# Performance work log

Measured on AMD Instinct MI355X. Metric: run time of the kernel, lower is better.

The kernel has to match this reference:

```python
import jax, jax.numpy as jnp
import numpy as np

NCONF, NATOMS, NCOEFF = 64, 256, 45
NAOV = 12  # 4 p-vectors + 8 d-vectors (3 'diagonal' + 5 'off-diagonal' rows)

# hyperparameters (floats from the forward signature, fixed here)
LOW_S, UP_S = 0.5, 3.5
LOW_R, UP_R = 0.5, 3.5
LOW_A, UP_A = 0.5, 3.5
LOW_Z, UP_Z = 0.19634954, 2.94524311  # ~pi/16 .. 15*pi/16
OETA_S, OETA_R, OETA_A, OZETA = 16.0, 16.0, 8.0, 32.0


def setup_inputs() -> dict:
    key = jax.random.key(0)
    coefficients = jax.random.normal(key, (NCONF, NATOMS, NCOEFF), dtype=jnp.float32)
    return {"coefficients": coefficients, "NOShfS": 16, "NOShfR": 16, "NOShfA": 8, "NOShfZ": 8}


def _orbital_matrix(coefficients):
    n, a, _ = coefficients.shape
    p = coefficients[:, :, 9:21].reshape(n, a, 4, 3)
    d = coefficients[:, :, 21:45].reshape(n, a, 4, 6)
    d = d[..., jnp.array([0, 2, 5, 4, 3, 1])].reshape(n, a, 8, 3)
    # cat([p, d[:, :, :3], d[:, :, 3:]]) == cat([p, d])
    return jnp.concatenate([p, d], axis=2)  # [n, a, 12, 3]


def reference(coefficients, NOShfS, NOShfR, NOShfA, NOShfZ):
    # basis_functions='spd', use_simple_orbital_aev=False, use_angular_info=True
    n, a, _ = coefficients.shape
    om = _orbital_matrix(coefficients)                 # [n, a, 12, 3]
    dist = jnp.linalg.norm(om, axis=-1)                # [n, a, 12]

    shfS = jnp.linspace(LOW_S, UP_S, NOShfS)
    shfR = jnp.linspace(LOW_R, UP_R, NOShfR)
    s_aev = jnp.exp(-OETA_S * (dist[..., None] - shfS) ** 2)   # [n, a, 12, S]
    r_aev = jnp.exp(-OETA_R * (dist[..., None] - shfR) ** 2)   # [n, a, 12, R]
    radial = jnp.concatenate([s_aev, r_aev], axis=-1).reshape(n, a, NAOV * (NOShfS + NOShfR))

    # angles between all AOV pairs (vectorized version of the nested i<j loop)
    zero_mask = jnp.all(jnp.abs(om) < 1e-12, axis=-1)          # [n, a, 12]
    safe_d = jnp.where(zero_mask, 1.0, dist)
    nv = jnp.where(zero_mask[..., None], 0.0, om / safe_d[..., None])  # normalized AOVs
    iu, ju = np.triu_indices(NAOV, k=1)                        # 66 pairs, i-major order
    cos_ang = jnp.einsum('napk,napk->nap', nv[:, :, iu], nv[:, :, ju])  # [n, a, 66]
    angles = jnp.arccos(0.95 * cos_ang)
    avdist = 0.5 * (dist[:, :, iu] + dist[:, :, ju])           # [n, a, 66]

    shfZ = jnp.linspace(LOW_Z, UP_Z, NOShfZ)
    shfA = jnp.linspace(LOW_A, UP_A, NOShfA)
    factor1 = ((1.0 + jnp.cos(angles[..., None] - shfZ)) * 0.5) ** OZETA      # [n, a, 66, Z]
    factor2 = jnp.exp(-OETA_A * (avdist[..., None] - shfA) ** 2)              # [n, a, 66, A]
    angular = 2.0 * factor1[..., :, None] * factor2[..., None, :]             # [n, a, 66, Z, A]
    angular = angular.reshape(n, a, angles.shape[2] * NOShfZ * NOShfA)

    return jnp.concatenate([radial, angular], axis=-1)  # [n, a, 12*(S+R) + 66*Z*A]
```

## Files before the change

### kernel.cpp

```cpp
#include <hip/hip_runtime.h>
#include <math.h>

#define NCONF  64
#define NATOMS 256
#define NCOEFF 45
#define NAOV   12
#define NPAIR  66
#define NZ     8
#define NA     8
#define RAD    384
#define ANG    4224
#define TOT    4608

__constant__ unsigned char c_iu[NPAIR] = {
    0,0,0,0,0,0,0,0,0,0,0,
    1,1,1,1,1,1,1,1,1,1,
    2,2,2,2,2,2,2,2,2,
    3,3,3,3,3,3,3,3,
    4,4,4,4,4,4,4,
    5,5,5,5,5,5,
    6,6,6,6,6,
    7,7,7,7,
    8,8,8,
    9,9,
    10
};
__constant__ unsigned char c_ju[NPAIR] = {
    1,2,3,4,5,6,7,8,9,10,11,
    2,3,4,5,6,7,8,9,10,11,
    3,4,5,6,7,8,9,10,11,
    4,5,6,7,8,9,10,11,
    5,6,7,8,9,10,11,
    6,7,8,9,10,11,
    7,8,9,10,11,
    8,9,10,11,
    9,10,11,
    10,11,
    11
};

__constant__ float c_shfS[16] = {
    0.5f, 0.7f, 0.9f, 1.1f, 1.3f, 1.5f, 1.7f, 1.9f,
    2.1f, 2.3f, 2.5f, 2.7f, 2.9f, 3.1f, 3.3f, 3.5f
};
__constant__ float c_shfA[8] = {
    0.5f, 0.92857142857f, 1.35714285714f, 1.78571428571f,
    2.21428571429f, 2.64285714286f, 3.07142857143f, 3.5f
};
__constant__ float c_cosZ[8] = {
     0.98078528f,  0.83146961f,  0.55557023f,  0.19509032f,
    -0.19509032f, -0.55557023f, -0.83146961f, -0.98078528f
};
__constant__ float c_sinZ[8] = {
    0.19509032f, 0.55557023f, 0.83146961f, 0.98078528f,
    0.98078528f, 0.83146961f, 0.55557023f, 0.19509032f
};


__global__ __launch_bounds__(256)
void OrbitalAEVComputer_40492951667225_kernel(const float* __restrict__ coef,
                                              float* __restrict__ out) {
    const int atom = blockIdx.x;
    const float* c = coef + (size_t)atom * NCOEFF;
    float* o = out + (size_t)atom * TOT;
    const int t = threadIdx.x;

    __shared__ float s_dist[NAOV];
    __shared__ float s_nv[NAOV][3];
    __shared__ float s_c95[NPAIR];
    __shared__ float s_sin[NPAIR];
    __shared__ float s_avd[NPAIR];
    __shared__ float s_f1[NPAIR * NZ];
    __shared__ float s_f2[NPAIR * NA];

    if (t < NAOV) {
        float x, y, z;
        if (t < 4) {
            x = c[9 + 3 * t]; y = c[10 + 3 * t]; z = c[11 + 3 * t];
        } else {
            int r = (t - 4) >> 1, h = (t - 4) & 1;
            const int base = 21 + 6 * r;
            if (h == 0) { x = c[base + 0]; y = c[base + 2]; z = c[base + 5]; }
            else        { x = c[base + 4]; y = c[base + 3]; z = c[base + 1]; }
        }
        float d = sqrtf(x * x + y * y + z * z);
        bool zm = (fabsf(x) < 1e-12f) && (fabsf(y) < 1e-12f) && (fabsf(z) < 1e-12f);
        float inv = zm ? 0.0f : 1.0f / d;
        s_dist[t] = d;
        s_nv[t][0] = x * inv;
        s_nv[t][1] = y * inv;
        s_nv[t][2] = z * inv;
    }
    __syncthreads();

    if (t < NPAIR) {
        int i = c_iu[t], j = c_ju[t];
        float cang = s_nv[i][0] * s_nv[j][0]
                   + s_nv[i][1] * s_nv[j][1]
                   + s_nv[i][2] * s_nv[j][2];
        float c95 = 0.95f * cang;
        s_c95[t] = c95;
        s_sin[t] = sqrtf(fmaxf(1.0f - c95 * c95, 0.0f));
        s_avd[t] = 0.5f * (s_dist[i] + s_dist[j]);
    }
    __syncthreads();

    for (int idx = t; idx < NPAIR * NZ; idx += 256) {
        int q = idx >> 3, k = idx & 7;
        float cosa = fmaf(s_c95[q], c_cosZ[k], s_sin[q] * c_sinZ[k]);
        float x = 0.5f * (1.0f + cosa);
        x = x * x; x = x * x; x = x * x; x = x * x; x = x * x;
        s_f1[idx] = x;
        float dd = s_avd[q] - c_shfA[k];
        s_f2[idx] = __expf(-8.0f * dd * dd);
    }
    __syncthreads();

    if (t < 96) {
        int e = t * 4;
        int p = e >> 5;
        float d = s_dist[p];
        int k0 = e & 31;
        float4 v;
        {
            float df = d - c_shfS[(k0 + 0) & 15]; v.x = __expf(-16.0f * df * df);
        }
        {
            float df = d - c_shfS[(k0 + 1) & 15]; v.y = __expf(-16.0f * df * df);
        }
        {
            float df = d - c_shfS[(k0 + 2) & 15]; v.z = __expf(-16.0f * df * df);
        }
        {
            float df = d - c_shfS[(k0 + 3) & 15]; v.w = __expf(-16.0f * df * df);
        }
        reinterpret_cast<float4*>(o)[t] = v;
    }

    for (int idx4 = t; idx4 < ANG / 4; idx4 += 256) {
        int e = idx4 * 4;
        int q = e >> 6;
        int z = (e >> 3) & 7;
        int a0 = e & 7;
        float f1 = 2.0f * s_f1[q * 8 + z];
        const float* f2 = &s_f2[q * 8 + a0];
        float4 v;
        v.x = f1 * f2[0];
        v.y = f1 * f2[1];
        v.z = f1 * f2[2];
        v.w = f1 * f2[3];
        reinterpret_cast<float4*>(o + RAD)[idx4] = v;
    }
}

extern "C" void kernel_launch(void* const* d_in, const int* in_sizes, int n_in,
                              void* d_out, int out_size, void* d_ws, size_t ws_size,
                              hipStream_t stream) {
    const float* coef = (const float*)d_in[0];
    float* out = (float*)d_out;
    OrbitalAEVComputer_40492951667225_kernel<<<dim3(NCONF * NATOMS), dim3(256), 0, stream>>>(coef, out);
}
```

Before: 312.1 us.

## Map one atom per wavefront and replace block barriers with wave-local LDS fences

Each 256-thread block now handles four atoms, one per 64-lane wavefront, with per-wave shared-memory slices. The block-wide __syncthreads calls are replaced by s_waitcnt lgkmcnt(0), relying on lockstep execution within a wavefront. The sine is recomputed per element rather than stored, and f2 is read as float4 from LDS. This removes block barrier overhead and idle threads in the small setup phases, but relies on implicit wave synchronicity and does more work per lane in the store loops.

After: 313.4 us. No clear change (+0.4%).

```diff
diff --git a/kernel.cpp b/kernel.cpp
--- a/kernel.cpp
+++ b/kernel.cpp
@@ -11,6 +11,7 @@
 #define RAD    384
 #define ANG    4224
 #define TOT    4608
+#define ATOMS_PER_BLOCK 4
 
 __constant__ unsigned char c_iu[NPAIR] = {
     0,0,0,0,0,0,0,0,0,0,0,
@@ -56,29 +57,32 @@
     0.98078528f, 0.83146961f, 0.55557023f, 0.19509032f
 };
 
+#define WAVE_FENCE() asm volatile("s_waitcnt lgkmcnt(0)" ::: "memory")
+
 
 __global__ __launch_bounds__(256)
 void OrbitalAEVComputer_40492951667225_kernel(const float* __restrict__ coef,
                                               float* __restrict__ out) {
-    const int atom = blockIdx.x;
+    __shared__ __align__(16) float s_f1[ATOMS_PER_BLOCK][NPAIR * NZ];
+    __shared__ __align__(16) float s_f2[ATOMS_PER_BLOCK][NPAIR * NA];
+    __shared__ float s_dist[ATOMS_PER_BLOCK][NAOV];
+    __shared__ float s_nv[ATOMS_PER_BLOCK][NAOV][3];
+    __shared__ float s_c95[ATOMS_PER_BLOCK][NPAIR];
+    __shared__ float s_avd[ATOMS_PER_BLOCK][NPAIR];
+
+    const int t = threadIdx.x;
+    const int w = t >> 6;
+    const int l = t & 63;
+    const int atom = blockIdx.x * ATOMS_PER_BLOCK + w;
     const float* c = coef + (size_t)atom * NCOEFF;
     float* o = out + (size_t)atom * TOT;
-    const int t = threadIdx.x;
 
-    __shared__ float s_dist[NAOV];
-    __shared__ float s_nv[NAOV][3];
-    __shared__ float s_c95[NPAIR];
-    __shared__ float s_sin[NPAIR];
-    __shared__ float s_avd[NPAIR];
-    __shared__ float s_f1[NPAIR * NZ];
-    __shared__ float s_f2[NPAIR * NA];
-
-    if (t < NAOV) {
+    if (l < NAOV) {
         float x, y, z;
-        if (t < 4) {
-            x = c[9 + 3 * t]; y = c[10 + 3 * t]; z = c[11 + 3 * t];
+        if (l < 4) {
+            x = c[9 + 3 * l]; y = c[10 + 3 * l]; z = c[11 + 3 * l];
         } else {
-            int r = (t - 4) >> 1, h = (t - 4) & 1;
+            int r = (l - 4) >> 1, h = (l - 4) & 1;
             const int base = 21 + 6 * r;
             if (h == 0) { x = c[base + 0]; y = c[base + 2]; z = c[base + 5]; }
             else        { x = c[base + 4]; y = c[base + 3]; z = c[base + 1]; }
@@ -86,70 +90,63 @@
         float d = sqrtf(x * x + y * y + z * z);
         bool zm = (fabsf(x) < 1e-12f) && (fabsf(y) < 1e-12f) && (fabsf(z) < 1e-12f);
         float inv = zm ? 0.0f : 1.0f / d;
-        s_dist[t] = d;
-        s_nv[t][0] = x * inv;
-        s_nv[t][1] = y * inv;
-        s_nv[t][2] = z * inv;
+        s_dist[w][l] = d;
+        s_nv[w][l][0] = x * inv;
+        s_nv[w][l][1] = y * inv;
+        s_nv[w][l][2] = z * inv;
     }
-    __syncthreads();
+    WAVE_FENCE();
 
-    if (t < NPAIR) {
-        int i = c_iu[t], j = c_ju[t];
-        float cang = s_nv[i][0] * s_nv[j][0]
-                   + s_nv[i][1] * s_nv[j][1]
-                   + s_nv[i][2] * s_nv[j][2];
-        float c95 = 0.95f * cang;
-        s_c95[t] = c95;
-        s_sin[t] = sqrtf(fmaxf(1.0f - c95 * c95, 0.0f));
-        s_avd[t] = 0.5f * (s_dist[i] + s_dist[j]);
+    for (int i4 = l; i4 < RAD / 4; i4 += 64) {
+        int e = i4 * 4;
+        int p = e >> 5;
+        float d = s_dist[w][p];
+        int k0 = e & 31;
+        float4 v;
+        float df;
+        df = d - c_shfS[(k0 + 0) & 15]; v.x = __expf(-16.0f * df * df);
+        df = d - c_shfS[(k0 + 1) & 15]; v.y = __expf(-16.0f * df * df);
+        df = d - c_shfS[(k0 + 2) & 15]; v.z = __expf(-16.0f * df * df);
+        df = d - c_shfS[(k0 + 3) & 15]; v.w = __expf(-16.0f * df * df);
+        reinterpret_cast<float4*>(o)[i4] = v;
     }
-    __syncthreads();
 
-    for (int idx = t; idx < NPAIR * NZ; idx += 256) {
+    for (int p = l; p < NPAIR; p += 64) {
+        int i = c_iu[p], j = c_ju[p];
+        float cang = s_nv[w][i][0] * s_nv[w][j][0]
+                   + s_nv[w][i][1] * s_nv[w][j][1]
+                   + s_nv[w][i][2] * s_nv[w][j][2];
+        s_c95[w][p] = 0.95f * cang;
+        s_avd[w][p] = 0.5f * (s_dist[w][i] + s_dist[w][j]);
+    }
+    WAVE_FENCE();
+
+    for (int idx = l; idx < NPAIR * NZ; idx += 64) {
         int q = idx >> 3, k = idx & 7;
-        float cosa = fmaf(s_c95[q], c_cosZ[k], s_sin[q] * c_sinZ[k]);
+        float c95 = s_c95[w][q];
+        float sinv = sqrtf(fmaxf(1.0f - c95 * c95, 0.0f));
+        float cosa = fmaf(c95, c_cosZ[k], sinv * c_sinZ[k]);
         float x = 0.5f * (1.0f + cosa);
         x = x * x; x = x * x; x = x * x; x = x * x; x = x * x;
-        s_f1[idx] = x;
-        float dd = s_avd[q] - c_shfA[k];
-        s_f2[idx] = __expf(-8.0f * dd * dd);
+        s_f1[w][idx] = x;
+        float dd = s_avd[w][q] - c_shfA[k];
+        s_f2[w][idx] = __expf(-8.0f * dd * dd);
     }
-    __syncthreads();
+    WAVE_FENCE();
 
-    if (t < 96) {
-        int e = t * 4;
-        int p = e >> 5;
-        float d = s_dist[p];
-        int k0 = e & 31;
+    float4* oa = reinterpret_cast<float4*>(o + RAD);
+    for (int i4 = l; i4 < ANG / 4; i4 += 64) {
+        int q  = i4 >> 4;
+        int z  = (i4 >> 1) & 7;
+        int a0 = (i4 & 1) * 4;
+        float f1 = 2.0f * s_f1[w][q * 8 + z];
+        float4 f2 = *reinterpret_cast<const float4*>(&s_f2[w][q * 8 + a0]);
         float4 v;
-        {
-            float df = d - c_shfS[(k0 + 0) & 15]; v.x = __expf(-16.0f * df * df);
-        }
-        {
-            float df = d - c_shfS[(k0 + 1) & 15]; v.y = __expf(-16.0f * df * df);
-        }
-        {
-            float df = d - c_shfS[(k0 + 2) & 15]; v.z = __expf(-16.0f * df * df);
-        }
-        {
-            float df = d - c_shfS[(k0 + 3) & 15]; v.w = __expf(-16.0f * df * df);
-        }
-        reinterpret_cast<float4*>(o)[t] = v;
-    }
-
-    for (int idx4 = t; idx4 < ANG / 4; idx4 += 256) {
-        int e = idx4 * 4;
-        int q = e >> 6;
-        int z = (e >> 3) & 7;
-        int a0 = e & 7;
-        float f1 = 2.0f * s_f1[q * 8 + z];
-        const float* f2 = &s_f2[q * 8 + a0];
-        float4 v;
-        v.x = f1 * f2[0];
-        v.y = f1 * f2[1];
-        v.z = f1 * f2[2];
-        v.w = f1 * f2[3];
-        reinterpret_cast<float4*>(o + RAD)[idx4] = v;
+        v.x = f1 * f2.x;
+        v.y = f1 * f2.y;
+        v.z = f1 * f2.z;
+        v.w = f1 * f2.w;
+        oa[i4] = v;
     }
 }
 
@@ -158,5 +155,6 @@
                               hipStream_t stream) {
     const float* coef = (const float*)d_in[0];
     float* out = (float*)d_out;
-    OrbitalAEVComputer_40492951667225_kernel<<<dim3(NCONF * NATOMS), dim3(256), 0, stream>>>(coef, out);
+    OrbitalAEVComputer_40492951667225_kernel<<<dim3(NCONF * NATOMS / ATOMS_PER_BLOCK),
+                                               dim3(256), 0, stream>>>(coef, out);
 }
```
